# Kernel optimization log

Measured on AMD Instinct MI355X. Metric: run time of the kernel, lower is better.

## Reference

```python
import jax, jax.numpy as jnp
import numpy as np

B, D, H, Q, N, V = 2048, 2048, 16, 128, 8192, 128


def setup_inputs() -> dict:
    key = jax.random.key(0)
    k1, k2, k3, k4, k5 = jax.random.split(key, 5)
    return {
        "x": jax.random.normal(k1, (B, D), dtype=jnp.float32),
        "keys": jax.random.normal(k2, (N, Q), dtype=jnp.float32),
        "values": jax.random.normal(k3, (N, V), dtype=jnp.float32),
        "Wq": jax.random.normal(k4, (H * Q, D), dtype=jnp.float32) * (1.0 / np.sqrt(D)),
        "Wo": jax.random.normal(k5, (D, H * V), dtype=jnp.float32) * (1.0 / np.sqrt(H * V)),
    }


def reference(x, keys, values, Wq, Wo):
    b = x.shape[0]
    h, q = H, Q
    # queries: [B, H, Q]
    queries = (x @ Wq.T).reshape(b, h, q)
    # einsum 'aib,ajb->aijb' then sum over last axis == dot product over Q
    scores = jnp.einsum('bhq,nq->bhn', queries, keys) / jnp.sqrt(jnp.asarray(q, x.dtype))
    attn = jax.nn.softmax(scores, axis=-1)  # [B, H, N]
    # Original: einsum('aib,ajc->aijc', attn, values) sums attn over its N axis
    # (label b) independently of values' N axis (label j), giving
    # out[a,i,j,c] = attn_rowsum[a,i] * values[j,c]; mean over j then yields
    # attn_rowsum[a,i] * mean_n(values)[c]. Computed here without the [B,H,N,V]
    # intermediate (mathematically identical).
    attn_rowsum = attn.sum(axis=-1)        # [B, H] (== 1 up to fp error)
    vmean = values.mean(axis=0)            # [V]
    outv = (attn_rowsum[:, :, None] * vmean[None, None, :]).reshape(b, -1)  # [B, H*V]
    return outv @ Wo.T + x
```

## Files before the change

kernel.cpp:

```cpp
#include <hip/hip_runtime.h>


#define NROWS 8192
#define VDIM  128
#define DDIM  2048
#define BDIM  2048
#define P_ROWS 128

__global__ void col_partial_kernel(const float4* __restrict__ vals4,
                                   float* __restrict__ partial) {
    __shared__ float4 s[256];
    const int t = threadIdx.x;
    const int b = blockIdx.x;
    float4 acc = make_float4(0.f, 0.f, 0.f, 0.f);
    const int base = b * 2048;
#pragma unroll
    for (int j = 0; j < 8; ++j) {
        float4 v = vals4[base + t + 256 * j];
        acc.x += v.x; acc.y += v.y; acc.z += v.z; acc.w += v.w;
    }
    s[t] = acc;
    __syncthreads();
    if (t < 32) {
        float4 r = s[t];
#pragma unroll
        for (int k = 1; k < 8; ++k) {
            float4 v = s[t + 32 * k];
            r.x += v.x; r.y += v.y; r.z += v.z; r.w += v.w;
        }
        float* p = partial + b * VDIM + t * 4;
        p[0] = r.x; p[1] = r.y; p[2] = r.z; p[3] = r.w;
    }
}

__global__ void compute_c_kernel(const float* __restrict__ partial,
                                 const float4* __restrict__ Wo4,
                                 float* __restrict__ cvec) {
    __shared__ float4 s[256];
    __shared__ float4 vm_lds[32];
    const int t = threadIdx.x;

    const float4* __restrict__ p4 = (const float4*)partial;
    float4 acc = make_float4(0.f, 0.f, 0.f, 0.f);
#pragma unroll
    for (int j = 0; j < 16; ++j) {
        float4 v = p4[t + 256 * j];
        acc.x += v.x; acc.y += v.y; acc.z += v.z; acc.w += v.w;
    }
    s[t] = acc;
    __syncthreads();
    if (t < 32) {
        float4 r = s[t];
#pragma unroll
        for (int k = 1; k < 8; ++k) {
            float4 v = s[t + 32 * k];
            r.x += v.x; r.y += v.y; r.z += v.z; r.w += v.w;
        }
        const float inv = 1.0f / (float)NROWS;
        r.x *= inv; r.y *= inv; r.z *= inv; r.w *= inv;
        vm_lds[t] = r;
    }
    __syncthreads();

    const int lane = t & 63;
    const int wave = t >> 6;
    const int d = blockIdx.x * 4 + wave;
    const float4 vm = vm_lds[lane & 31];
    const float4* row = Wo4 + (size_t)d * 512;
    float dot = 0.f;
#pragma unroll
    for (int i = 0; i < 8; ++i) {
        float4 w = row[i * 64 + lane];
        dot += w.x * vm.x + w.y * vm.y + w.z * vm.z + w.w * vm.w;
    }
#pragma unroll
    for (int off = 32; off; off >>= 1) dot += __shfl_down(dot, off);
    if (lane == 0) cvec[d] = dot;
}

__global__ void add_bias_kernel(const float4* __restrict__ x4,
                                const float* __restrict__ cvec,
                                float4* __restrict__ out4) {
    const float4* __restrict__ c4 = (const float4*)cvec;
    const int n4 = (BDIM * DDIM) / 4;
    int idx = blockIdx.x * blockDim.x + threadIdx.x;
    const int stride = gridDim.x * blockDim.x;
    for (int i = idx; i < n4; i += stride) {
        float4 xv = x4[i];
        float4 cv = c4[i & 511];
        xv.x += cv.x; xv.y += cv.y; xv.z += cv.z; xv.w += cv.w;
        out4[i] = xv;
    }
}

extern "C" void kernel_launch(void* const* d_in, const int* in_sizes, int n_in,
                              void* d_out, int out_size, void* d_ws, size_t ws_size,
                              hipStream_t stream) {
    const float* x      = (const float*)d_in[0];
    const float* values = (const float*)d_in[2];
    const float* Wo     = (const float*)d_in[4];
    float* out = (float*)d_out;
    float* ws  = (float*)d_ws;

    float* partial = ws;
    float* cvec    = ws + P_ROWS * VDIM;

    col_partial_kernel<<<P_ROWS, 256, 0, stream>>>((const float4*)values, partial);
    compute_c_kernel<<<512, 256, 0, stream>>>(partial, (const float4*)Wo, cvec);
    add_bias_kernel<<<1024, 256, 0, stream>>>((const float4*)x, cvec, (float4*)out);
}
```

Baseline: 21.35 us.

## Fold Wo over heads in prep kernel and fuse c-vector with bias add

Values column partials and a head-folded Wo (summing the 16 head slices into a D x 128 matrix) are now produced in one prep kernel. The c-vector dot products are then computed per block from the folded Wo and used directly in the x+c add. This drops one kernel launch and the cvec round trip through global memory. In exchange each of the 1024 blocks redundantly reduces the partials and recomputes 128 dot products.

```diff
diff --git a/kernel.cpp b/kernel.cpp
--- a/kernel.cpp
+++ b/kernel.cpp
@@ -7,44 +7,73 @@
 #define BDIM  2048
 #define P_ROWS 128
 
-__global__ void col_partial_kernel(const float4* __restrict__ vals4,
-                                   float* __restrict__ partial) {
+__global__ void prep_kernel(const float4* __restrict__ vals4,
+                            const float4* __restrict__ Wo4,
+                            float4* __restrict__ partial4,
+                            float4* __restrict__ WoF4) {
     __shared__ float4 s[256];
     const int t = threadIdx.x;
     const int b = blockIdx.x;
-    float4 acc = make_float4(0.f, 0.f, 0.f, 0.f);
-    const int base = b * 2048;
+
+    if (b < P_ROWS) {
+        float4 acc = make_float4(0.f, 0.f, 0.f, 0.f);
+        const int base = b * 2048;
 #pragma unroll
-    for (int j = 0; j < 8; ++j) {
-        float4 v = vals4[base + t + 256 * j];
-        acc.x += v.x; acc.y += v.y; acc.z += v.z; acc.w += v.w;
-    }
-    s[t] = acc;
-    __syncthreads();
-    if (t < 32) {
-        float4 r = s[t];
+        for (int j = 0; j < 8; ++j) {
+            float4 v = vals4[base + t + 256 * j];
+            acc.x += v.x; acc.y += v.y; acc.z += v.z; acc.w += v.w;
+        }
+        s[t] = acc;
+        __syncthreads();
+        if (t < 32) {
+            float4 r = s[t];
 #pragma unroll
-        for (int k = 1; k < 8; ++k) {
-            float4 v = s[t + 32 * k];
-            r.x += v.x; r.y += v.y; r.z += v.z; r.w += v.w;
+            for (int k = 1; k < 8; ++k) {
+                float4 v = s[t + 32 * k];
+                r.x += v.x; r.y += v.y; r.z += v.z; r.w += v.w;
+            }
+            partial4[b * 32 + t] = r;
         }
-        float* p = partial + b * VDIM + t * 4;
-        p[0] = r.x; p[1] = r.y; p[2] = r.z; p[3] = r.w;
+    } else {
+        const int wb = b - P_ROWS;
+        const int vq = t & 31;
+        const int hg = t >> 5;
+        for (int d = wb; d < DDIM; d += 896) {
+            const float4* row = Wo4 + (size_t)d * 512;
+            float4 a = row[(2 * hg) * 32 + vq];
+            float4 c = row[(2 * hg + 1) * 32 + vq];
+            a.x += c.x; a.y += c.y; a.z += c.z; a.w += c.w;
+            s[t] = a;
+            __syncthreads();
+            if (t < 32) {
+                float4 r = s[t];
+#pragma unroll
+                for (int k = 1; k < 8; ++k) {
+                    float4 v = s[t + 32 * k];
+                    r.x += v.x; r.y += v.y; r.z += v.z; r.w += v.w;
+                }
+                WoF4[d * 32 + t] = r;
+            }
+            __syncthreads();
+        }
     }
 }
 
-__global__ void compute_c_kernel(const float* __restrict__ partial,
-                                 const float4* __restrict__ Wo4,
-                                 float* __restrict__ cvec) {
+__global__ void c_add_kernel(const float4* __restrict__ partial4,
+                             const float4* __restrict__ WoF4,
+                             const float4* __restrict__ x4,
+                             float4* __restrict__ out4) {
     __shared__ float4 s[256];
     __shared__ float4 vm_lds[32];
+    __shared__ float  c_lds[128];
     const int t = threadIdx.x;
+    const int dc = blockIdx.x & 15;
+    const int rg = blockIdx.x >> 4;
 
-    const float4* __restrict__ p4 = (const float4*)partial;
     float4 acc = make_float4(0.f, 0.f, 0.f, 0.f);
 #pragma unroll
     for (int j = 0; j < 16; ++j) {
-        float4 v = p4[t + 256 * j];
+        float4 v = partial4[t + 256 * j];
         acc.x += v.x; acc.y += v.y; acc.z += v.z; acc.w += v.w;
     }
     s[t] = acc;
@@ -62,34 +91,33 @@
     }
     __syncthreads();
 
-    const int lane = t & 63;
-    const int wave = t >> 6;
-    const int d = blockIdx.x * 4 + wave;
-    const float4 vm = vm_lds[lane & 31];
-    const float4* row = Wo4 + (size_t)d * 512;
-    float dot = 0.f;
+    {
+        const int ld = t >> 1;
+        const int half = t & 1;
+        const size_t base = (size_t)(dc * 128 + ld) * 32 + half * 16;
+        float dot = 0.f;
 #pragma unroll
-    for (int i = 0; i < 8; ++i) {
-        float4 w = row[i * 64 + lane];
-        dot += w.x * vm.x + w.y * vm.y + w.z * vm.z + w.w * vm.w;
+        for (int j = 0; j < 16; ++j) {
+            float4 w = WoF4[base + j];
+            float4 vm = vm_lds[half * 16 + j];
+            dot += w.x * vm.x + w.y * vm.y + w.z * vm.z + w.w * vm.w;
+        }
+        dot += __shfl_xor(dot, 1);
+        if (half == 0) c_lds[ld] = dot;
     }
+    __syncthreads();
+
+    const float4* __restrict__ c4 = (const float4*)c_lds;
+    const int q = t & 31;
+    const int r0 = rg * 32 + (t >> 5);
+    const float4 cv = c4[q];
 #pragma unroll
-    for (int off = 32; off; off >>= 1) dot += __shfl_down(dot, off);
-    if (lane == 0) cvec[d] = dot;
-}
-
-__global__ void add_bias_kernel(const float4* __restrict__ x4,
-                                const float* __restrict__ cvec,
-                                float4* __restrict__ out4) {
-    const float4* __restrict__ c4 = (const float4*)cvec;
-    const int n4 = (BDIM * DDIM) / 4;
-    int idx = blockIdx.x * blockDim.x + threadIdx.x;
-    const int stride = gridDim.x * blockDim.x;
-    for (int i = idx; i < n4; i += stride) {
-        float4 xv = x4[i];
-        float4 cv = c4[i & 511];
+    for (int i = 0; i < 4; ++i) {
+        const int r = r0 + i * 8;
+        const size_t idx = (size_t)r * 512 + dc * 32 + q;
+        float4 xv = x4[idx];
         xv.x += cv.x; xv.y += cv.y; xv.z += cv.z; xv.w += cv.w;
-        out4[i] = xv;
+        out4[idx] = xv;
     }
 }
 
@@ -102,10 +130,11 @@
     float* out = (float*)d_out;
     float* ws  = (float*)d_ws;
 
-    float* partial = ws;
-    float* cvec    = ws + P_ROWS * VDIM;
+    float4* partial4 = (float4*)ws;
+    float4* WoF4     = (float4*)(ws + P_ROWS * VDIM);
 
-    col_partial_kernel<<<P_ROWS, 256, 0, stream>>>((const float4*)values, partial);
-    compute_c_kernel<<<512, 256, 0, stream>>>(partial, (const float4*)Wo, cvec);
-    add_bias_kernel<<<1024, 256, 0, stream>>>((const float4*)x, cvec, (float4*)out);
+    prep_kernel<<<1024, 256, 0, stream>>>((const float4*)values, (const float4*)Wo,
+                                          partial4, WoF4);
+    c_add_kernel<<<1024, 256, 0, stream>>>(partial4, WoF4,
+                                           (const float4*)x, (float4*)out);
 }
```

New measurement: 24.59 us. +15.2%, slower.
